# Kernel optimization log

Hardware: AMD Instinct MI355X
Metric: run time of the kernel (lower is better)

## Reference

```python
import jax, jax.numpy as jnp
import numpy as np

H = 16      # num_attention_heads
D = 128     # head_size
ROT = 32    # rotary_ndims
WIN = 256   # attention_window[layer_id]
G = 64      # max_global_tokens
BASE = 10000.0


def _rotate_half(x):
    x1, x2 = jnp.split(x, 2, axis=-1)
    return jnp.concatenate([-x2, x1], axis=-1)


def setup_inputs() -> dict:
    key = jax.random.key(0)
    ks = jax.random.split(key, 6)
    B, S, HD = 2, 2048, H * D
    hidden_states = jax.random.normal(ks[0], (B, S, HD), jnp.float32)
    attention_mask = jnp.zeros((B, 1, 1, S), jnp.float32)
    glob_idx = jnp.sort(jax.random.randint(ks[1], (B, G), 0, S), axis=-1)
    W_qkv = jax.random.normal(ks[2], (HD, 3 * HD), jnp.float32) * 0.02
    b_qkv = jnp.zeros((3 * HD,), jnp.float32)
    W_o = jax.random.normal(ks[3], (HD, HD), jnp.float32) * 0.02
    b_o = jnp.zeros((HD,), jnp.float32)
    return {"hidden_states": hidden_states, "attention_mask": attention_mask,
            "glob_idx": glob_idx, "W_qkv": W_qkv, "b_qkv": b_qkv,
            "W_o": W_o, "b_o": b_o}


def reference(hidden_states, attention_mask, glob_idx, W_qkv, b_qkv, W_o, b_o):
    B, S, HD = hidden_states.shape
    qkv = (hidden_states @ W_qkv + b_qkv).reshape(B, S, H, 3 * D)
    q = qkv[..., :D].transpose(0, 2, 1, 3)        # [B,H,S,D]
    k = qkv[..., D:2 * D].transpose(0, 2, 1, 3)
    v = qkv[..., 2 * D:].transpose(0, 2, 1, 3)

    # GPT-NeoX rotary on first ROT dims
    inv_freq = 1.0 / (BASE ** (jnp.arange(0, ROT, 2, dtype=jnp.float32) / ROT))
    freqs = jnp.einsum('s,f->sf', jnp.arange(S, dtype=jnp.float32), inv_freq)
    emb = jnp.concatenate([freqs, freqs], axis=-1)           # [S,ROT]
    cos = jnp.cos(emb)[None, None]
    sin = jnp.sin(emb)[None, None]
    q = jnp.concatenate([q[..., :ROT] * cos + _rotate_half(q[..., :ROT]) * sin,
                         q[..., ROT:]], axis=-1)
    k = jnp.concatenate([k[..., :ROT] * cos + _rotate_half(k[..., :ROT]) * sin,
                         k[..., ROT:]], axis=-1)

    # step_attn path: keys/values are head-averaged before attention (key.mean(1))
    k_mean = k.mean(axis=1)   # [B,S,D]
    v_mean = v.mean(axis=1)
    scale = 1.0 / jnp.sqrt(jnp.float32(D))
    minv = jnp.finfo(jnp.float32).min

    s0 = jnp.einsum('bhqd,bkd->bhqk', q[:, :, :WIN], k_mean[:, :WIN]) * scale
    causal = jnp.tril(jnp.ones((WIN, WIN), bool))
    s0 = jnp.where(causal[None, None], s0, minv) + attention_mask[..., :WIN]
    out0 = jnp.einsum('bhqk,bkd->bhqd', jax.nn.softmax(s0, axis=-1), v_mean[:, :WIN])

    Sq = S - WIN
    steps = jnp.arange(Sq)
    win_pos = steps[:, None] + 1 + jnp.arange(WIN)[None, :]
    k_win = k_mean[:, win_pos]
    v_win = v_mean[:, win_pos]
    mask_win = attention_mask[:, 0, 0, :][:, win_pos][:, None]
    qs = q[:, :, WIN:]                                        # [B,H,Sq,D]
    s_win = jnp.einsum('bhqd,bqwd->bhqw', qs, k_win) * scale + mask_win

    k_glob = jnp.take_along_axis(k_mean, glob_idx[..., None], axis=1)  # [B,G,D]
    v_glob = jnp.take_along_axis(v_mean, glob_idx[..., None], axis=1)
    # sorted indices: 'filter < i then truncate to G' == prefix-valid mask per slot
    valid = (glob_idx[:, None, :] < steps[None, :, None])[:, None]     # [B,1,Sq,G]
    s_glob = jnp.where(valid, jnp.einsum('bhqd,bgd->bhqg', qs, k_glob) * scale, minv)

    w = jax.nn.softmax(jnp.concatenate([s_glob, s_win], axis=-1), axis=-1)
    out_steps = (jnp.einsum('bhqg,bgd->bhqd', w[..., :G], v_glob)
                 + jnp.einsum('bhqw,bqwd->bhqd', w[..., G:], v_win))

    out = jnp.concatenate([out0, out_steps], axis=2)          # [B,H,S,D]
    out = out.transpose(0, 2, 1, 3).reshape(B, S, HD)
    return out @ W_o + b_o
```

## Files before the change

### kernel.cpp

```cpp
#include <hip/hip_runtime.h>
#include <math.h>

#define SCALE_ 0.08838834764831845f
#define MINV_  (-3.4028234663852886e38f)

typedef __bf16 bf16;
typedef bf16  bf16x4 __attribute__((ext_vector_type(4)));
typedef bf16  bf16x8 __attribute__((ext_vector_type(8)));
typedef float f32x4  __attribute__((ext_vector_type(4)));
typedef float float4v __attribute__((ext_vector_type(4)));

#define LD8(p) (*(const bf16x8*)(p))

__device__ __forceinline__ f32x4 mfma16(bf16x8 a, bf16x8 b, f32x4 c) {
    return __builtin_amdgcn_mfma_f32_16x16x32_bf16(a, b, c, 0, 0, 0);
}

typedef const __attribute__((address_space(1))) void* gas_t;
typedef __attribute__((address_space(3))) void* sas_t;
__device__ __forceinline__ void gload_lds16(const void* g, void* l) {
    __builtin_amdgcn_global_load_lds((gas_t)g, (sas_t)l, 16, 0, 0);
}


__global__ __launch_bounds__(256) void cast_hidden_kernel(const float* __restrict__ X, bf16* __restrict__ Y)
{
    int i = (blockIdx.x * 256 + threadIdx.x) * 4;
    float4v v = *(const float4v*)(X + i);
    bf16x4 o; o.x = (bf16)v.x; o.y = (bf16)v.y; o.z = (bf16)v.z; o.w = (bf16)v.w;
    *(bf16x4*)(Y + i) = o;
}

__global__ __launch_bounds__(256) void transpose_cast_kernel(const float* __restrict__ W, bf16* __restrict__ BT,
                                                             int srcStride, int qmap)
{
    __shared__ float tile[32][33];
    int k0 = blockIdx.x * 32, n0 = blockIdx.y * 32;
    int c = threadIdx.x & 31, r = threadIdx.x >> 5;
    int n = n0 + c;
    int src = qmap ? ((n >> 7) * 384 + (n & 127)) : n;
    #pragma unroll
    for (int rr = 0; rr < 32; rr += 8)
        tile[r + rr][c] = W[(size_t)(k0 + r + rr) * srcStride + src];
    __syncthreads();
    #pragma unroll
    for (int rr = 0; rr < 32; rr += 8)
        BT[(size_t)(n0 + r + rr) * 2048 + k0 + c] = (bf16)tile[c][r + rr];
}

__global__ __launch_bounds__(256) void bt1_kv_kernel(const float* __restrict__ Wqkv, bf16* __restrict__ BT1)
{
    int k0 = blockIdx.x * 16;
    int j = threadIdx.x;
    float acc[16];
    #pragma unroll
    for (int k = 0; k < 16; k++) acc[k] = 0.f;
    for (int h = 0; h < 16; h++) {
        #pragma unroll
        for (int k = 0; k < 16; k++)
            acc[k] += Wqkv[(size_t)(k0 + k) * 6144 + h * 384 + 128 + j];
    }
    #pragma unroll
    for (int k = 0; k < 16; k++)
        BT1[(size_t)(2048 + j) * 2048 + k0 + k] = (bf16)(acc[k] * 0.0625f);
}

__global__ void bias1_kernel(const float* __restrict__ bqkv, float* __restrict__ bias1)
{
    int c = blockIdx.x * 256 + threadIdx.x;
    if (c >= 2304) return;
    if (c < 2048) bias1[c] = bqkv[(c >> 7) * 384 + (c & 127)];
    else {
        int j = c - 2048; float s = 0.f;
        for (int h = 0; h < 16; h++) s += bqkv[h * 384 + 128 + j];
        bias1[c] = s * 0.0625f;
    }
}

template<int OUT_BF16>
__global__ __launch_bounds__(256) void gemm_kernel(const bf16* __restrict__ A, const bf16* __restrict__ BT,
                                                   const float* __restrict__ bias, void* __restrict__ Cout,
                                                   int M, int N, int K)
{
    __shared__ __align__(16) bf16 As[128 * 64];
    __shared__ __align__(16) bf16 Bs[128 * 64];
    const int tid  = threadIdx.x;
    const int wv   = tid >> 6, lane = tid & 63, quad = lane >> 4, l16 = lane & 15;
    const int wrow = wv >> 1, wcol = wv & 1;
    const int m0 = blockIdx.y * 128, n0 = blockIdx.x * 128;

    int rowS[4], colS[4];
    #pragma unroll
    for (int j = 0; j < 4; j++) {
        int flat = (wv * 4 + j) * 64 + lane;
        int row = flat >> 3, cp = flat & 7;
        rowS[j] = row;
        colS[j] = (cp ^ (row & 7)) * 8;
    }

    f32x4 acc[4][4];
    #pragma unroll
    for (int i = 0; i < 4; i++)
        #pragma unroll
        for (int j = 0; j < 4; j++) acc[i][j] = (f32x4){0.f, 0.f, 0.f, 0.f};

    for (int kk = 0; kk < K; kk += 64) {
        __syncthreads();
        #pragma unroll
        for (int j = 0; j < 4; j++) {
            gload_lds16(A  + (size_t)(m0 + rowS[j]) * K + kk + colS[j], &As[(wv * 4 + j) * 512]);
            gload_lds16(BT + (size_t)(n0 + rowS[j]) * K + kk + colS[j], &Bs[(wv * 4 + j) * 512]);
        }
        __syncthreads();

        bf16x8 af[4][2], bfr[4][2];
        #pragma unroll
        for (int i = 0; i < 4; i++) {
            int row = wrow * 64 + i * 16 + l16;
            #pragma unroll
            for (int ks = 0; ks < 2; ks++) {
                int lc = ks * 4 + quad;
                af[i][ks] = LD8(&As[row * 64 + ((lc ^ (row & 7)) * 8)]);
            }
        }
        #pragma unroll
        for (int i = 0; i < 4; i++) {
            int row = wcol * 64 + i * 16 + l16;
            #pragma unroll
            for (int ks = 0; ks < 2; ks++) {
                int lc = ks * 4 + quad;
                bfr[i][ks] = LD8(&Bs[row * 64 + ((lc ^ (row & 7)) * 8)]);
            }
        }
        #pragma unroll
        for (int ks = 0; ks < 2; ks++)
            #pragma unroll
            for (int i = 0; i < 4; i++)
                #pragma unroll
                for (int j = 0; j < 4; j++)
                    acc[i][j] = mfma16(af[i][ks], bfr[j][ks], acc[i][j]);
    }

    #pragma unroll
    for (int i = 0; i < 4; i++) {
        #pragma unroll
        for (int j = 0; j < 4; j++) {
            int n = n0 + wcol * 64 + j * 16 + l16;
            float bn = bias[n];
            #pragma unroll
            for (int r = 0; r < 4; r++) {
                int m = m0 + wrow * 64 + i * 16 + quad * 4 + r;
                float v = acc[i][j][r] + bn;
                if (OUT_BF16) ((bf16*)Cout)[(size_t)m * N + n] = (bf16)v;
                else          ((float*)Cout)[(size_t)m * N + n] = v;
            }
        }
    }
}

__global__ __launch_bounds__(320) void rotary_kernel(bf16* __restrict__ C1)
{
    int row = blockIdx.x;
    int s = row & 2047;
    int t = threadIdx.x;
    if (t >= 272) return;
    int g = t >> 4, dd = t & 15;
    bf16* ptr = C1 + (size_t)row * 2304 + (g < 16 ? g * 128 : 2048);
    float x0 = (float)ptr[dd], x1 = (float)ptr[dd + 16];
    const float L = 0.575646273248511f;
    float inv = expf(-L * (float)dd);
    float ang = (float)s * inv;
    float c = cosf(ang), si = sinf(ang);
    ptr[dd]      = (bf16)(x0 * c - x1 * si);
    ptr[dd + 16] = (bf16)(x1 * c + x0 * si);
}

__global__ __launch_bounds__(256) void build_vmT_kernel(const bf16* __restrict__ C1, bf16* __restrict__ vmT)
{
    __shared__ float tile[32][33];
    int b = blockIdx.z;
    int s0 = blockIdx.x * 32, d0 = blockIdx.y * 32;
    int c = threadIdx.x & 31, r = threadIdx.x >> 5;
    #pragma unroll
    for (int rr = 0; rr < 32; rr += 8)
        tile[r + rr][c] = (float)C1[(size_t)(b * 2048 + s0 + r + rr) * 2304 + 2176 + d0 + c];
    __syncthreads();
    #pragma unroll
    for (int rr = 0; rr < 32; rr += 8)
        vmT[(size_t)(b * 128 + d0 + r + rr) * 2048 + s0 + c] = (bf16)tile[c][r + rr];
}

__global__ __launch_bounds__(256) void pretile_win_kernel(const bf16* __restrict__ C1, const bf16* __restrict__ vmT,
                                                          bf16* __restrict__ KF, bf16* __restrict__ VF)
{
    int c = blockIdx.x, b = blockIdx.y;
    for (int i = 0; i < 8; i++) {
        int sid = threadIdx.x + i * 256;
        int lane = sid & 63, fi = (sid >> 6) & 15;
        int l16 = lane & 15, quad = lane >> 4;
        if (sid < 1024) {
            int t = fi >> 2, ks = fi & 3;
            const bf16* src = C1 + (size_t)(b * 2048 + c * 64 + t * 16 + l16) * 2304 + 2048 + ks * 32 + quad * 8;
            *(bf16x8*)&KF[((size_t)(b * 33 + c) * 16 + fi) * 512 + lane * 8] = LD8(src);
        } else {
            int dt = fi >> 1, ks2 = fi & 1;
            const bf16* src = vmT + (size_t)(b * 128 + dt * 16 + l16) * 2048 + c * 64 + ks2 * 32 + quad * 8;
            *(bf16x8*)&VF[((size_t)(b * 33 + c) * 16 + fi) * 512 + lane * 8] = LD8(src);
        }
    }
}

__global__ __launch_bounds__(256) void pretile_glob_kernel(const bf16* __restrict__ C1, const bf16* __restrict__ vmT,
                                                           const int* __restrict__ gidx,
                                                           bf16* __restrict__ KF, bf16* __restrict__ VF)
{
    int b = blockIdx.x;
    for (int i = 0; i < 8; i++) {
        int sid = threadIdx.x + i * 256;
        int lane = sid & 63, fi = (sid >> 6) & 15;
        int l16 = lane & 15, quad = lane >> 4;
        if (sid < 1024) {
            int t = fi >> 2, ks = fi & 3;
            int pos = gidx[b * 64 + t * 16 + l16];
            const bf16* src = C1 + (size_t)(b * 2048 + pos) * 2304 + 2048 + ks * 32 + quad * 8;
            *(bf16x8*)&KF[((size_t)(b * 33 + 32) * 16 + fi) * 512 + lane * 8] = LD8(src);
        } else {
            int dt = fi >> 1, ks2 = fi & 1;
            int d = dt * 16 + l16;
            bf16 tmp[8];
            #pragma unroll
            for (int j = 0; j < 8; j++) {
                int pos = gidx[b * 64 + ks2 * 32 + quad * 8 + j];
                tmp[j] = vmT[(size_t)(b * 128 + d) * 2048 + pos];
            }
            #pragma unroll
            for (int j = 0; j < 8; j++)
                VF[((size_t)(b * 33 + 32) * 16 + fi) * 512 + lane * 8 + j] = tmp[j];
        }
    }
}

#define PSTRIDE 88

__global__ __launch_bounds__(256) void attn0_kernel(const bf16* __restrict__ C1, const bf16* __restrict__ KF,
                                                    const bf16* __restrict__ VF, const float* __restrict__ mask,
                                                    bf16* __restrict__ attn)
{
    const int bx = blockIdx.x, h = blockIdx.y, b = blockIdx.z;
    const int tid = threadIdx.x, wv = tid >> 6, lane = tid & 63, quad = lane >> 4, l16 = lane & 15;
    const int q0 = (bx * 4 + wv) * 16;

    __shared__ __align__(16) bf16 Ps[4 * 16 * PSTRIDE];
    bf16* Pw = &Ps[wv * (16 * PSTRIDE)];

    bf16x8 af[4];
    const bf16* qbase = C1 + (size_t)(b * 2048 + q0 + l16) * 2304 + h * 128;
    #pragma unroll
    for (int ks = 0; ks < 4; ks++) af[ks] = LD8(qbase + ks * 32 + quad * 8);

    f32x4 m_run = (f32x4){MINV_, MINV_, MINV_, MINV_};
    f32x4 l_run = (f32x4){0.f, 0.f, 0.f, 0.f};
    f32x4 O[8];
    #pragma unroll
    for (int dt = 0; dt < 8; dt++) O[dt] = (f32x4){0.f, 0.f, 0.f, 0.f};

    for (int c = 0; c <= bx; c++) {
        const bf16* KFc = KF + ((size_t)(b * 33 + c) * 16) * 512;
        const bf16* VFc = VF + ((size_t)(b * 33 + c) * 16) * 512;

        f32x4 acc[4];
        #pragma unroll
        for (int t = 0; t < 4; t++) acc[t] = (f32x4){0.f, 0.f, 0.f, 0.f};
        #pragma unroll
        for (int t = 0; t < 4; t++)
            #pragma unroll
            for (int ks = 0; ks < 4; ks++)
                acc[t] = mfma16(af[ks], LD8(KFc + (size_t)(t * 4 + ks) * 512 + lane * 8), acc[t]);

        float sv[4][4];
        #pragma unroll
        for (int t = 0; t < 4; t++) {
            int key = c * 64 + t * 16 + l16;
            float addv = mask[b * 2048 + key];
            #pragma unroll
            for (int r = 0; r < 4; r++) {
                int q = q0 + quad * 4 + r;
                sv[t][r] = (key <= q) ? (acc[t][r] * SCALE_ + addv) : MINV_;
            }
        }

        f32x4 cm;
        #pragma unroll
        for (int r = 0; r < 4; r++) cm[r] = fmaxf(fmaxf(sv[0][r], sv[1][r]), fmaxf(sv[2][r], sv[3][r]));
        #pragma unroll
        for (int ms = 1; ms < 16; ms <<= 1)
            #pragma unroll
            for (int r = 0; r < 4; r++) cm[r] = fmaxf(cm[r], __shfl_xor(cm[r], ms, 64));

        f32x4 nm, alpha;
        #pragma unroll
        for (int r = 0; r < 4; r++) { nm[r] = fmaxf(m_run[r], cm[r]); alpha[r] = __expf(m_run[r] - nm[r]); }

        float pv[4][4];
        f32x4 cs = (f32x4){0.f, 0.f, 0.f, 0.f};
        #pragma unroll
        for (int t = 0; t < 4; t++)
            #pragma unroll
            for (int r = 0; r < 4; r++) {
                pv[t][r] = __expf(sv[t][r] - nm[r]);
                cs[r] += pv[t][r];
            }
        #pragma unroll
        for (int ms = 1; ms < 16; ms <<= 1)
            #pragma unroll
            for (int r = 0; r < 4; r++) cs[r] += __shfl_xor(cs[r], ms, 64);

        m_run = nm;
        #pragma unroll
        for (int r = 0; r < 4; r++) l_run[r] = l_run[r] * alpha[r] + cs[r];
        #pragma unroll
        for (int dt = 0; dt < 8; dt++)
            #pragma unroll
            for (int r = 0; r < 4; r++) O[dt][r] *= alpha[r];

        #pragma unroll
        for (int t = 0; t < 4; t++)
            #pragma unroll
            for (int r = 0; r < 4; r++)
                Pw[(quad * 4 + r) * PSTRIDE + t * 16 + l16] = (bf16)pv[t][r];
        bf16x8 pa0 = LD8(&Pw[l16 * PSTRIDE + quad * 8]);
        bf16x8 pa1 = LD8(&Pw[l16 * PSTRIDE + 32 + quad * 8]);

        #pragma unroll
        for (int dt = 0; dt < 8; dt++) {
            O[dt] = mfma16(pa0, LD8(VFc + (size_t)(dt * 2 + 0) * 512 + lane * 8), O[dt]);
            O[dt] = mfma16(pa1, LD8(VFc + (size_t)(dt * 2 + 1) * 512 + lane * 8), O[dt]);
        }
    }

    f32x4 invl;
    #pragma unroll
    for (int r = 0; r < 4; r++) invl[r] = 1.0f / l_run[r];
    #pragma unroll
    for (int dt = 0; dt < 8; dt++)
        #pragma unroll
        for (int r = 0; r < 4; r++) {
            int q = q0 + quad * 4 + r;
            attn[(size_t)(b * 2048 + q) * 2048 + h * 128 + dt * 16 + l16] = (bf16)(O[dt][r] * invl[r]);
        }
}

__global__ __launch_bounds__(256) void attn_steps3_kernel(const bf16* __restrict__ C1, const bf16* __restrict__ KF,
                                                          const bf16* __restrict__ VF, const float* __restrict__ mask,
                                                          const int* __restrict__ gidx, bf16* __restrict__ attn)
{
    const int sb = blockIdx.x, b = blockIdx.y;
    const int tid = threadIdx.x, wv = tid >> 6, lane = tid & 63, quad = lane >> 4, l16 = lane & 15;
    const int step = sb * 4 + wv, p = 256 + step;

    __shared__ __align__(16) bf16 Ps[4 * 16 * PSTRIDE];
    bf16* Pw = &Ps[wv * (16 * PSTRIDE)];

    bf16x8 af[4];
    const bf16* qrow = C1 + (size_t)(b * 2048 + p) * 2304;
    #pragma unroll
    for (int ks = 0; ks < 4; ks++) af[ks] = LD8(qrow + l16 * 128 + ks * 32 + quad * 8);

    int gix[4];
    #pragma unroll
    for (int t = 0; t < 4; t++) gix[t] = gidx[b * 64 + t * 16 + l16];

    f32x4 m_run = (f32x4){MINV_, MINV_, MINV_, MINV_};
    f32x4 l_run = (f32x4){0.f, 0.f, 0.f, 0.f};
    f32x4 O[8];
    #pragma unroll
    for (int dt = 0; dt < 8; dt++) O[dt] = (f32x4){0.f, 0.f, 0.f, 0.f};

    const int c0 = (step + 1) >> 6;

    for (int iter = 0; iter < 6; iter++) {
        int c;
        bool isGlob = (iter == 0);
        if (isGlob) c = 32;
        else { c = c0 + iter - 1; if (c > 31) break; }

        const bf16* KFc = KF + ((size_t)(b * 33 + c) * 16) * 512;
        const bf16* VFc = VF + ((size_t)(b * 33 + c) * 16) * 512;

        f32x4 acc[4];
        #pragma unroll
        for (int t = 0; t < 4; t++) acc[t] = (f32x4){0.f, 0.f, 0.f, 0.f};
        #pragma unroll
        for (int t = 0; t < 4; t++)
            #pragma unroll
            for (int ks = 0; ks < 4; ks++)
                acc[t] = mfma16(af[ks], LD8(KFc + (size_t)(t * 4 + ks) * 512 + lane * 8), acc[t]);

        float sv[4][4];
        bool vld[4];
        #pragma unroll
        for (int t = 0; t < 4; t++) {
            float addv = 0.f;
            if (isGlob) vld[t] = gix[t] < step;
            else {
                int pos = c * 64 + t * 16 + l16;
                vld[t] = (unsigned)(pos - step - 1) < 256u;
                addv = mask[b * 2048 + pos];
            }
            #pragma unroll
            for (int r = 0; r < 4; r++) sv[t][r] = vld[t] ? (acc[t][r] * SCALE_ + addv) : MINV_;
        }

        f32x4 cm;
        #pragma unroll
        for (int r = 0; r < 4; r++) cm[r] = fmaxf(fmaxf(sv[0][r], sv[1][r]), fmaxf(sv[2][r], sv[3][r]));
        #pragma unroll
        for (int ms = 1; ms < 16; ms <<= 1)
            #pragma unroll
            for (int r = 0; r < 4; r++) cm[r] = fmaxf(cm[r], __shfl_xor(cm[r], ms, 64));

        f32x4 nm, alpha;
        #pragma unroll
        for (int r = 0; r < 4; r++) { nm[r] = fmaxf(m_run[r], cm[r]); alpha[r] = __expf(m_run[r] - nm[r]); }

        float pv[4][4];
        f32x4 cs = (f32x4){0.f, 0.f, 0.f, 0.f};
        #pragma unroll
        for (int t = 0; t < 4; t++)
            #pragma unroll
            for (int r = 0; r < 4; r++) {
                pv[t][r] = vld[t] ? __expf(sv[t][r] - nm[r]) : 0.f;
                cs[r] += pv[t][r];
            }
        #pragma unroll
        for (int ms = 1; ms < 16; ms <<= 1)
            #pragma unroll
            for (int r = 0; r < 4; r++) cs[r] += __shfl_xor(cs[r], ms, 64);

        m_run = nm;
        #pragma unroll
        for (int r = 0; r < 4; r++) l_run[r] = l_run[r] * alpha[r] + cs[r];
        #pragma unroll
        for (int dt = 0; dt < 8; dt++)
            #pragma unroll
            for (int r = 0; r < 4; r++) O[dt][r] *= alpha[r];

        #pragma unroll
        for (int t = 0; t < 4; t++)
            #pragma unroll
            for (int r = 0; r < 4; r++)
                Pw[(quad * 4 + r) * PSTRIDE + t * 16 + l16] = (bf16)pv[t][r];
        bf16x8 pa0 = LD8(&Pw[l16 * PSTRIDE + quad * 8]);
        bf16x8 pa1 = LD8(&Pw[l16 * PSTRIDE + 32 + quad * 8]);

        #pragma unroll
        for (int dt = 0; dt < 8; dt++) {
            O[dt] = mfma16(pa0, LD8(VFc + (size_t)(dt * 2 + 0) * 512 + lane * 8), O[dt]);
            O[dt] = mfma16(pa1, LD8(VFc + (size_t)(dt * 2 + 1) * 512 + lane * 8), O[dt]);
        }
    }

    f32x4 invl;
    #pragma unroll
    for (int r = 0; r < 4; r++) invl[r] = 1.0f / l_run[r];
    #pragma unroll
    for (int dt = 0; dt < 8; dt++)
        #pragma unroll
        for (int r = 0; r < 4; r++) {
            int h = quad * 4 + r;
            attn[(size_t)(b * 2048 + p) * 2048 + h * 128 + dt * 16 + l16] = (bf16)(O[dt][r] * invl[r]);
        }
}

extern "C" void kernel_launch(void* const* d_in, const int* in_sizes, int n_in,
                              void* d_out, int out_size, void* d_ws, size_t ws_size,
                              hipStream_t stream)
{
    const float* hidden = (const float*)d_in[0];
    const float* amask  = (const float*)d_in[1];
    const int*   gidx   = (const int*)d_in[2];
    const float* Wqkv   = (const float*)d_in[3];
    const float* bqkv   = (const float*)d_in[4];
    const float* Wo     = (const float*)d_in[5];
    const float* bo     = (const float*)d_in[6];

    char* ws = (char*)d_ws;
    size_t off = 0;
    auto take = [&](size_t bytes) -> char* {
        char* p = ws + off;
        off = (off + bytes + 255) & ~(size_t)255;
        return p;
    };
    bf16*  A16   = (bf16*)take(4096ull * 2048 * 2);
    bf16*  BT1   = (bf16*)take(2304ull * 2048 * 2);
    bf16*  BT2   = (bf16*)take(2048ull * 2048 * 2);
    bf16*  C1    = (bf16*)take(4096ull * 2304 * 2);
    bf16*  vmT   = (bf16*)take(2ull * 128 * 2048 * 2);
    bf16*  KF    = (bf16*)take(2ull * 33 * 16 * 512 * 2);
    bf16*  VF    = (bf16*)take(2ull * 33 * 16 * 512 * 2);
    bf16*  attnb = (bf16*)take(4096ull * 2048 * 2);
    float* bias1 = (float*)take(2304 * 4);

    cast_hidden_kernel<<<8192, 256, 0, stream>>>(hidden, A16);
    transpose_cast_kernel<<<dim3(64, 64), 256, 0, stream>>>(Wqkv, BT1, 6144, 1);
    bt1_kv_kernel<<<128, 256, 0, stream>>>(Wqkv, BT1);
    bias1_kernel<<<9, 256, 0, stream>>>(bqkv, bias1);
    transpose_cast_kernel<<<dim3(64, 64), 256, 0, stream>>>(Wo, BT2, 2048, 0);

    gemm_kernel<1><<<dim3(18, 32), 256, 0, stream>>>(A16, BT1, bias1, (void*)C1, 4096, 2304, 2048);

    rotary_kernel<<<4096, 320, 0, stream>>>(C1);
    build_vmT_kernel<<<dim3(64, 4, 2), 256, 0, stream>>>(C1, vmT);
    pretile_win_kernel<<<dim3(32, 2), 256, 0, stream>>>(C1, vmT, KF, VF);
    pretile_glob_kernel<<<2, 256, 0, stream>>>(C1, vmT, gidx, KF, VF);

    attn0_kernel<<<dim3(4, 16, 2), 256, 0, stream>>>(C1, KF, VF, amask, attnb);
    attn_steps3_kernel<<<dim3(448, 2), 256, 0, stream>>>(C1, KF, VF, amask, gidx, attnb);

    gemm_kernel<0><<<dim3(16, 32), 256, 0, stream>>>(attnb, BT2, bo, d_out, 4096, 2048, 2048);

    (void)in_sizes; (void)n_in; (void)out_size; (void)ws_size;
}
```

Baseline: 327.2 us.

## Use 32x32x16 MFMA in GEMM, fast sincos in rotary, merge pretile kernels

The GEMM inner loop moves from 16x16x32 MFMA tiles to 32x32x16 MFMA tiles, so each wave holds 2x2 accumulators of 16 floats instead of 4x4 of 4. This cuts LDS fragment loads per MFMA and the instruction count, but changes the epilogue store pattern. Separately, the rotary kernel switches to the fast __expf/__sincosf intrinsics, which lose some accuracy. The window and global pretile kernels are merged into a single launch to save one launch.

```diff
diff --git a/kernel.cpp b/kernel.cpp
--- a/kernel.cpp
+++ b/kernel.cpp
@@ -8,12 +8,16 @@
 typedef bf16  bf16x4 __attribute__((ext_vector_type(4)));
 typedef bf16  bf16x8 __attribute__((ext_vector_type(8)));
 typedef float f32x4  __attribute__((ext_vector_type(4)));
+typedef float f32x16 __attribute__((ext_vector_type(16)));
 typedef float float4v __attribute__((ext_vector_type(4)));
 
 #define LD8(p) (*(const bf16x8*)(p))
 
 __device__ __forceinline__ f32x4 mfma16(bf16x8 a, bf16x8 b, f32x4 c) {
     return __builtin_amdgcn_mfma_f32_16x16x32_bf16(a, b, c, 0, 0, 0);
+}
+__device__ __forceinline__ f32x16 mfma32(bf16x8 a, bf16x8 b, f32x16 c) {
+    return __builtin_amdgcn_mfma_f32_32x32x16_bf16(a, b, c, 0, 0, 0);
 }
 
 typedef const __attribute__((address_space(1))) void* gas_t;
@@ -85,7 +89,7 @@
     __shared__ __align__(16) bf16 As[128 * 64];
     __shared__ __align__(16) bf16 Bs[128 * 64];
     const int tid  = threadIdx.x;
-    const int wv   = tid >> 6, lane = tid & 63, quad = lane >> 4, l16 = lane & 15;
+    const int wv   = tid >> 6, lane = tid & 63, l32 = lane & 31, half = lane >> 5;
     const int wrow = wv >> 1, wcol = wv & 1;
     const int m0 = blockIdx.y * 128, n0 = blockIdx.x * 128;
 
@@ -98,11 +102,13 @@
         colS[j] = (cp ^ (row & 7)) * 8;
     }
 
-    f32x4 acc[4][4];
-    #pragma unroll
-    for (int i = 0; i < 4; i++)
-        #pragma unroll
-        for (int j = 0; j < 4; j++) acc[i][j] = (f32x4){0.f, 0.f, 0.f, 0.f};
+    f32x16 acc[2][2];
+    #pragma unroll
+    for (int i = 0; i < 2; i++)
+        #pragma unroll
+        for (int j = 0; j < 2; j++)
+            #pragma unroll
+            for (int r = 0; r < 16; r++) acc[i][j][r] = 0.f;
 
     for (int kk = 0; kk < K; kk += 64) {
         __syncthreads();
@@ -113,44 +119,44 @@
         }
         __syncthreads();
 
-        bf16x8 af[4][2], bfr[4][2];
-        #pragma unroll
-        for (int i = 0; i < 4; i++) {
-            int row = wrow * 64 + i * 16 + l16;
-            #pragma unroll
-            for (int ks = 0; ks < 2; ks++) {
-                int lc = ks * 4 + quad;
-                af[i][ks] = LD8(&As[row * 64 + ((lc ^ (row & 7)) * 8)]);
-            }
-        }
-        #pragma unroll
-        for (int i = 0; i < 4; i++) {
-            int row = wcol * 64 + i * 16 + l16;
-            #pragma unroll
-            for (int ks = 0; ks < 2; ks++) {
-                int lc = ks * 4 + quad;
-                bfr[i][ks] = LD8(&Bs[row * 64 + ((lc ^ (row & 7)) * 8)]);
-            }
-        }
-        #pragma unroll
-        for (int ks = 0; ks < 2; ks++)
-            #pragma unroll
-            for (int i = 0; i < 4; i++)
+        bf16x8 af[2][4], bfr[2][4];
+        #pragma unroll
+        for (int mt = 0; mt < 2; mt++) {
+            int row = wrow * 64 + mt * 32 + l32;
+            #pragma unroll
+            for (int k16 = 0; k16 < 4; k16++) {
+                int lc = k16 * 2 + half;
+                af[mt][k16] = LD8(&As[row * 64 + ((lc ^ (row & 7)) * 8)]);
+            }
+        }
+        #pragma unroll
+        for (int nt = 0; nt < 2; nt++) {
+            int row = wcol * 64 + nt * 32 + l32;
+            #pragma unroll
+            for (int k16 = 0; k16 < 4; k16++) {
+                int lc = k16 * 2 + half;
+                bfr[nt][k16] = LD8(&Bs[row * 64 + ((lc ^ (row & 7)) * 8)]);
+            }
+        }
+        #pragma unroll
+        for (int k16 = 0; k16 < 4; k16++)
+            #pragma unroll
+            for (int mt = 0; mt < 2; mt++)
                 #pragma unroll
-                for (int j = 0; j < 4; j++)
-                    acc[i][j] = mfma16(af[i][ks], bfr[j][ks], acc[i][j]);
-    }
-
-    #pragma unroll
-    for (int i = 0; i < 4; i++) {
-        #pragma unroll
-        for (int j = 0; j < 4; j++) {
-            int n = n0 + wcol * 64 + j * 16 + l16;
+                for (int nt = 0; nt < 2; nt++)
+                    acc[mt][nt] = mfma32(af[mt][k16], bfr[nt][k16], acc[mt][nt]);
+    }
+
+    #pragma unroll
+    for (int mt = 0; mt < 2; mt++) {
+        #pragma unroll
+        for (int nt = 0; nt < 2; nt++) {
+            int n = n0 + wcol * 64 + nt * 32 + l32;
             float bn = bias[n];
             #pragma unroll
-            for (int r = 0; r < 4; r++) {
-                int m = m0 + wrow * 64 + i * 16 + quad * 4 + r;
-                float v = acc[i][j][r] + bn;
+            for (int r = 0; r < 16; r++) {
+                int m = m0 + wrow * 64 + mt * 32 + (r & 3) + 8 * (r >> 2) + 4 * half;
+                float v = acc[mt][nt][r] + bn;
                 if (OUT_BF16) ((bf16*)Cout)[(size_t)m * N + n] = (bf16)v;
                 else          ((float*)Cout)[(size_t)m * N + n] = v;
             }
@@ -168,9 +174,10 @@
     bf16* ptr = C1 + (size_t)row * 2304 + (g < 16 ? g * 128 : 2048);
     float x0 = (float)ptr[dd], x1 = (float)ptr[dd + 16];
     const float L = 0.575646273248511f;
-    float inv = expf(-L * (float)dd);
+    float inv = __expf(-L * (float)dd);
     float ang = (float)s * inv;
-    float c = cosf(ang), si = sinf(ang);
+    float c, si;
+    __sincosf(ang, &si, &c);
     ptr[dd]      = (bf16)(x0 * c - x1 * si);
     ptr[dd + 16] = (bf16)(x1 * c + x0 * si);
 }
@@ -190,52 +197,38 @@
         vmT[(size_t)(b * 128 + d0 + r + rr) * 2048 + s0 + c] = (bf16)tile[c][r + rr];
 }
 
-__global__ __launch_bounds__(256) void pretile_win_kernel(const bf16* __restrict__ C1, const bf16* __restrict__ vmT,
-                                                          bf16* __restrict__ KF, bf16* __restrict__ VF)
+__global__ __launch_bounds__(256) void pretile_kernel(const bf16* __restrict__ C1, const bf16* __restrict__ vmT,
+                                                      const int* __restrict__ gidx,
+                                                      bf16* __restrict__ KF, bf16* __restrict__ VF)
 {
     int c = blockIdx.x, b = blockIdx.y;
+    bool isGlob = (c == 32);
     for (int i = 0; i < 8; i++) {
         int sid = threadIdx.x + i * 256;
         int lane = sid & 63, fi = (sid >> 6) & 15;
         int l16 = lane & 15, quad = lane >> 4;
         if (sid < 1024) {
             int t = fi >> 2, ks = fi & 3;
-            const bf16* src = C1 + (size_t)(b * 2048 + c * 64 + t * 16 + l16) * 2304 + 2048 + ks * 32 + quad * 8;
+            int pos = isGlob ? gidx[b * 64 + t * 16 + l16] : (c * 64 + t * 16 + l16);
+            const bf16* src = C1 + (size_t)(b * 2048 + pos) * 2304 + 2048 + ks * 32 + quad * 8;
             *(bf16x8*)&KF[((size_t)(b * 33 + c) * 16 + fi) * 512 + lane * 8] = LD8(src);
         } else {
             int dt = fi >> 1, ks2 = fi & 1;
-            const bf16* src = vmT + (size_t)(b * 128 + dt * 16 + l16) * 2048 + c * 64 + ks2 * 32 + quad * 8;
-            *(bf16x8*)&VF[((size_t)(b * 33 + c) * 16 + fi) * 512 + lane * 8] = LD8(src);
-        }
-    }
-}
-
-__global__ __launch_bounds__(256) void pretile_glob_kernel(const bf16* __restrict__ C1, const bf16* __restrict__ vmT,
-                                                           const int* __restrict__ gidx,
-                                                           bf16* __restrict__ KF, bf16* __restrict__ VF)
-{
-    int b = blockIdx.x;
-    for (int i = 0; i < 8; i++) {
-        int sid = threadIdx.x + i * 256;
-        int lane = sid & 63, fi = (sid >> 6) & 15;
-        int l16 = lane & 15, quad = lane >> 4;
-        if (sid < 1024) {
-            int t = fi >> 2, ks = fi & 3;
-            int pos = gidx[b * 64 + t * 16 + l16];
-            const bf16* src = C1 + (size_t)(b * 2048 + pos) * 2304 + 2048 + ks * 32 + quad * 8;
-            *(bf16x8*)&KF[((size_t)(b * 33 + 32) * 16 + fi) * 512 + lane * 8] = LD8(src);
-        } else {
-            int dt = fi >> 1, ks2 = fi & 1;
             int d = dt * 16 + l16;
-            bf16 tmp[8];
-            #pragma unroll
-            for (int j = 0; j < 8; j++) {
-                int pos = gidx[b * 64 + ks2 * 32 + quad * 8 + j];
-                tmp[j] = vmT[(size_t)(b * 128 + d) * 2048 + pos];
-            }
-            #pragma unroll
-            for (int j = 0; j < 8; j++)
-                VF[((size_t)(b * 33 + 32) * 16 + fi) * 512 + lane * 8 + j] = tmp[j];
+            if (isGlob) {
+                bf16 tmp[8];
+                #pragma unroll
+                for (int j = 0; j < 8; j++) {
+                    int pos = gidx[b * 64 + ks2 * 32 + quad * 8 + j];
+                    tmp[j] = vmT[(size_t)(b * 128 + d) * 2048 + pos];
+                }
+                #pragma unroll
+                for (int j = 0; j < 8; j++)
+                    VF[((size_t)(b * 33 + 32) * 16 + fi) * 512 + lane * 8 + j] = tmp[j];
+            } else {
+                const bf16* src = vmT + (size_t)(b * 128 + d) * 2048 + c * 64 + ks2 * 32 + quad * 8;
+                *(bf16x8*)&VF[((size_t)(b * 33 + c) * 16 + fi) * 512 + lane * 8] = LD8(src);
+            }
         }
     }
 }
@@ -511,8 +504,7 @@
 
     rotary_kernel<<<4096, 320, 0, stream>>>(C1);
     build_vmT_kernel<<<dim3(64, 4, 2), 256, 0, stream>>>(C1, vmT);
-    pretile_win_kernel<<<dim3(32, 2), 256, 0, stream>>>(C1, vmT, KF, VF);
-    pretile_glob_kernel<<<2, 256, 0, stream>>>(C1, vmT, gidx, KF, VF);
+    pretile_kernel<<<dim3(33, 2), 256, 0, stream>>>(C1, vmT, gidx, KF, VF);
 
     attn0_kernel<<<dim3(4, 16, 2), 256, 0, stream>>>(C1, KF, VF, amask, attnb);
     attn_steps3_kernel<<<dim3(448, 2), 256, 0, stream>>>(C1, KF, VF, amask, gidx, attnb);
```

After: 321.0 us. About the same (-1.9%).
